# Kernel optimization log

Hardware: AMD Instinct MI355X
Metric: run time of the kernel (lower is better)

## Reference

```python
import jax, jax.numpy as jnp
import numpy as np

B, N, D, H = 4, 2048, 1024, 16
DH = D // H


def setup_inputs() -> dict:
    key = jax.random.key(0)
    ks = jax.random.split(key, 9)
    std = 0.02
    return {
        "x": jax.random.normal(ks[0], (B, N, D), dtype=jnp.float32),
        "Wq": jax.random.normal(ks[1], (D, D), dtype=jnp.float32) * std,
        "bq": jnp.zeros((D,), dtype=jnp.float32),
        "Wk": jax.random.normal(ks[2], (D, D), dtype=jnp.float32) * std,
        "bk": jnp.zeros((D,), dtype=jnp.float32),
        "Wv": jax.random.normal(ks[3], (D, D), dtype=jnp.float32) * std,
        "bv": jnp.zeros((D,), dtype=jnp.float32),
        "Wo": jax.random.normal(ks[4], (D, D), dtype=jnp.float32) * std,
        "bo": jnp.zeros((D,), dtype=jnp.float32),
        "k": 8,
        "dilation": 2,
    }


def _dilated_mask(n_q, n_k, k, dilation):
    # allowed[i, j] = True iff |j - i| <= k*dilation and (j - i) % dilation == 0
    i = jnp.arange(n_q)[:, None]
    j = jnp.arange(n_k)[None, :]
    d = j - i
    return (jnp.abs(d) <= k * dilation) & ((d % dilation) == 0)


def reference(x, Wq, bq, Wk, bk, Wv, bv, Wo, bo, k, dilation):
    b, n_q, d_model = x.shape
    n_heads = H
    d_head = d_model // n_heads
    # self-attention: context = x
    q = (x @ Wq + bq).reshape(b, n_q, n_heads, d_head).transpose(0, 2, 1, 3)  # (B,H,Nq,Dh)
    kk = (x @ Wk + bk).reshape(b, n_q, n_heads, d_head).transpose(0, 2, 1, 3)
    v = (x @ Wv + bv).reshape(b, n_q, n_heads, d_head).transpose(0, 2, 1, 3)

    scale = 1.0 / np.sqrt(d_head).astype(np.float32)
    scores = jnp.einsum("bhqd,bhkd->bhqk", q, kk) * scale  # (B,H,Nq,Nk)
    allowed = _dilated_mask(n_q, n_q, k, dilation)  # (Nq,Nk)
    scores = jnp.where(allowed[None, None], scores, -jnp.inf)
    attn = jax.nn.softmax(scores, axis=-1)
    out = jnp.einsum("bhqk,bhkd->bhqd", attn, v)  # (B,H,Nq,Dh)
    out = out.transpose(0, 2, 1, 3).reshape(b, n_q, d_model)
    return out @ Wo + bo
```

## Files before the change

kernel.cpp:

```cpp
#include <hip/hip_runtime.h>
#include <hip/hip_bf16.h>
#include <hip/hip_fp16.h>
#include <stdint.h>

using bf16 = __hip_bfloat16;

typedef __bf16    bf16x8 __attribute__((ext_vector_type(8)));
typedef float     floatx4 __attribute__((ext_vector_type(4)));
typedef _Float16  f16x8 __attribute__((ext_vector_type(8)));

typedef __attribute__((address_space(3))) void as3_void;
typedef __attribute__((address_space(1))) void as1_void;

#define GLD_LDS16(gp, lp) \
  __builtin_amdgcn_global_load_lds((as1_void*)(uintptr_t)(gp), (as3_void*)(uintptr_t)(lp), 16, 0, 0)

#define FENCE() asm volatile("" ::: "memory")
#define BAR()   do { FENCE(); __builtin_amdgcn_s_barrier(); FENCE(); } while (0)
#define PIN()   __builtin_amdgcn_sched_barrier(0)

__global__ __launch_bounds__(256) void prep_kernel(
    const float* __restrict__ x,
    const float* __restrict__ Wq, const float* __restrict__ Wk,
    const float* __restrict__ Wv, const float* __restrict__ Wo,
    bf16* __restrict__ xbf, bf16* __restrict__ WTqkv, bf16* __restrict__ WoT) {
  __shared__ float tile[64 * 68];
  const int blk = blockIdx.x;
  const int tid = threadIdx.x;
  if (blk < 1024) {
    const int z = blk >> 8, t = blk & 255;
    const float* src = (z == 0) ? Wq : (z == 1) ? Wk : (z == 2) ? Wv : Wo;
    bf16* dst = (z < 3) ? (WTqkv + (size_t)z * 1024 * 1024) : WoT;
    const int nbase = (t & 15) * 64, kbase = (t >> 4) * 64;
    const int r1 = tid >> 4, c1 = tid & 15;
#pragma unroll
    for (int it = 0; it < 4; ++it) {
      const int row = r1 + it * 16;
      const float4 v = *(const float4*)(src + (size_t)(kbase + row) * 1024 + nbase + c1 * 4);
      *(float4*)(tile + row * 68 + c1 * 4) = v;
    }
    __syncthreads();
    const int c2 = tid & 7, n2 = tid >> 3;
#pragma unroll
    for (int it2 = 0; it2 < 2; ++it2) {
      const int n = n2 + it2 * 32;
      bf16 o[8];
#pragma unroll
      for (int s = 0; s < 8; ++s) o[s] = (bf16)tile[(8 * c2 + s) * 68 + n];
      *(uint4*)(dst + (size_t)(nbase + n) * 1024 + kbase + 8 * c2) = *(const uint4*)o;
    }
  } else {
    const size_t basei = ((size_t)(blk - 1024) * 256 + tid) * 16;
#pragma unroll
    for (int h = 0; h < 2; ++h) {
      const float4 a = *(const float4*)(x + basei + h * 8);
      const float4 b = *(const float4*)(x + basei + h * 8 + 4);
      bf16 o[8] = {(bf16)a.x, (bf16)a.y, (bf16)a.z, (bf16)a.w,
                   (bf16)b.x, (bf16)b.y, (bf16)b.z, (bf16)b.w};
      *(uint4*)(xbf + basei + h * 8) = *(const uint4*)o;
    }
  }
}

#define SAU(bufi, u, kt) \
  GLD_LDS16(A + abase + (uint64_t)(u) * 65536 + (uint64_t)(kt) * 64, \
            (char*)Asp[bufi] + (u) * 8192 + ldst)
#define SBU(bufi, u, kt) \
  GLD_LDS16(Bt + bbase + (uint64_t)(u) * 65536 + (uint64_t)(kt) * 64, \
            (char*)Bsp[bufi] + (u) * 8192 + ldst)

#define RDA2(bufi, mb) do { \
    const char* _p = (const char*)Asp[bufi] + (wm * 64 + (mb) * 16 + l16) * 128; \
    af[0][0] = *(const bf16x8*)(_p + pcb0); \
    af[0][1] = *(const bf16x8*)(_p + pcb1); \
    af[1][0] = *(const bf16x8*)(_p + 2048 + pcb0); \
    af[1][1] = *(const bf16x8*)(_p + 2048 + pcb1); \
  } while (0)

#define RDB6(bufi) do { \
    const char* _p = (const char*)Bsp[bufi] + (wn * 96 + l16) * 128; \
    _Pragma("unroll") for (int _j = 0; _j < 6; ++_j) { \
      bfr[_j][0] = *(const bf16x8*)(_p + _j * 2048 + pcb0); \
      bfr[_j][1] = *(const bf16x8*)(_p + _j * 2048 + pcb1); \
    } \
  } while (0)

#define MMQ24(mb) do { \
    _Pragma("unroll") for (int _i = 0; _i < 2; ++_i) \
      _Pragma("unroll") for (int _j = 0; _j < 6; ++_j) \
        _Pragma("unroll") for (int _k = 0; _k < 2; ++_k) \
          acc[(mb) + _i][_j] = __builtin_amdgcn_mfma_f32_16x16x32_bf16( \
              af[_i][_k], bfr[_j][_k], acc[(mb) + _i][_j], 0, 0, 0); \
  } while (0)

__global__ __launch_bounds__(512, 2) void gemm_qkv_8ph(
    const bf16* __restrict__ A, const bf16* __restrict__ Bt,
    const float* __restrict__ b0, const float* __restrict__ b1, const float* __restrict__ b2,
    __half* __restrict__ qkv) {
  const int t    = threadIdx.x;
  const int m0   = blockIdx.x * 256;
  const int n0   = blockIdx.y * 192;
  const int lane = t & 63;
  const int wave = t >> 6;
  const int wm   = wave >> 1;
  const int wn   = wave & 1;
  const int quad = lane >> 4;
  const int l16  = lane & 15;

  __shared__ alignas(16) char smem[114688];
  bf16* const Asp[2] = {(bf16*)smem, (bf16*)(smem + 32768)};
  bf16* const Bsp[2] = {(bf16*)(smem + 65536), (bf16*)(smem + 90112)};

  const int srt = t >> 3;
  const int sct = ((t & 7) ^ (srt & 7)) << 3;
  const uint64_t abase = (uint64_t)(m0 + srt) * 1024 + sct;
  const uint64_t bbase = (uint64_t)(n0 + srt) * 1024 + sct;
  const int ldst = t * 16;

  const int pcb0 = ((quad) ^ (l16 & 7)) << 4;
  const int pcb1 = ((4 + quad) ^ (l16 & 7)) << 4;

  floatx4 acc[4][6];
#pragma unroll
  for (int i = 0; i < 4; ++i)
#pragma unroll
    for (int j = 0; j < 6; ++j) {
      floatx4 z = {0.f, 0.f, 0.f, 0.f};
      acc[i][j] = z;
    }
  bf16x8 af[2][2], bfr[6][2];

  SBU(0, 0, 0); SBU(0, 1, 0); SBU(0, 2, 0);
  SAU(0, 0, 0); SAU(0, 1, 0); SAU(0, 2, 0); SAU(0, 3, 0);
  SBU(1, 0, 1); SBU(1, 1, 1); SBU(1, 2, 1);
  asm volatile("s_waitcnt vmcnt(3)" ::: "memory");
  BAR();

  for (int i = 0; i < 8; ++i) {
    const int kt1 = 2 * i + 1;
    const int kt2 = 2 * i + 2;
    const int kt3 = 2 * i + 3;
    const bool pf = (i < 7);

    RDA2(0, 0); RDB6(0);
    SAU(1, 0, kt1); SAU(1, 1, kt1); SAU(1, 2, kt1); SAU(1, 3, kt1);
    __builtin_amdgcn_s_setprio(1); MMQ24(0); __builtin_amdgcn_s_setprio(0);
    PIN();
    BAR();

    RDA2(0, 2);
    if (pf) { SBU(0, 0, kt2); SBU(0, 1, kt2); SBU(0, 2, kt2); }
    __builtin_amdgcn_s_setprio(1); MMQ24(2); __builtin_amdgcn_s_setprio(0);
    PIN();
    if (pf) { asm volatile("s_waitcnt vmcnt(3)" ::: "memory"); }
    else    { asm volatile("s_waitcnt vmcnt(0)" ::: "memory"); }
    BAR();

    RDA2(1, 0); RDB6(1);
    if (pf) { SAU(0, 0, kt2); SAU(0, 1, kt2); SAU(0, 2, kt2); SAU(0, 3, kt2); }
    __builtin_amdgcn_s_setprio(1); MMQ24(0); __builtin_amdgcn_s_setprio(0);
    PIN();
    BAR();

    RDA2(1, 2);
    if (pf) { SBU(1, 0, kt3); SBU(1, 1, kt3); SBU(1, 2, kt3); }
    __builtin_amdgcn_s_setprio(1); MMQ24(2); __builtin_amdgcn_s_setprio(0);
    PIN();
    if (pf) { asm volatile("s_waitcnt vmcnt(3)" ::: "memory"); }
    BAR();
  }

  float bvs[6];
#pragma unroll
  for (int nj = 0; nj < 6; ++nj) {
    const int n = n0 + wn * 96 + nj * 16 + l16;
    const int which = n >> 10;
    const int c = n & 1023;
    bvs[nj] = ((which == 0) ? b0 : (which == 1) ? b1 : b2)[c];
  }
  _Float16* stg = (_Float16*)smem;
#pragma unroll
  for (int mb = 0; mb < 4; ++mb)
#pragma unroll
    for (int nj = 0; nj < 6; ++nj)
#pragma unroll
      for (int r = 0; r < 4; ++r)
        stg[(wm * 64 + mb * 16 + quad * 4 + r) * 200 + wn * 96 + nj * 16 + l16] =
            (_Float16)(acc[mb][nj][r] + bvs[nj]);
  BAR();
#pragma unroll
  for (int rep = 0; rep < 12; ++rep) {
    const int cc = t + rep * 512;
    const int rl = cc / 24;
    const int ch = cc - rl * 24;
    const f16x8 v = *(const f16x8*)(stg + rl * 200 + ch * 8);
    *(f16x8*)((_Float16*)qkv + (size_t)(m0 + rl) * 3072 + n0 + ch * 8) = v;
  }
}

__global__ __launch_bounds__(256) void gemm_proj(
    const bf16* __restrict__ A, const bf16* __restrict__ Bt,
    const float* __restrict__ bias, float* __restrict__ fout) {
  const int tid  = threadIdx.x;
  const int m0   = blockIdx.x * 128;
  const int n0   = blockIdx.y * 128;
  const int lane = tid & 63;
  const int wave = tid >> 6;
  const int wr   = (wave >> 1) * 64;
  const int wc   = (wave & 1) * 64;
  const int quad = lane >> 4;
  const int l16  = lane & 15;

  __shared__ alignas(16) bf16 As[128 * 64];
  __shared__ alignas(16) bf16 Bs[128 * 64];

  const int srow = tid >> 3;
  const int cg   = (tid & 7) ^ (srow & 7);
  const uint64_t aoff = (uint64_t)(m0 + srow) * 1024 + cg * 8;
  const uint64_t boff = (uint64_t)(n0 + srow) * 1024 + cg * 8;

  floatx4 acc[4][4];
#pragma unroll
  for (int i = 0; i < 4; ++i)
#pragma unroll
    for (int j = 0; j < 4; ++j) {
      floatx4 z = {0.f, 0.f, 0.f, 0.f};
      acc[i][j] = z;
    }

  for (int k0 = 0; k0 < 1024; k0 += 64) {
    __syncthreads();
#pragma unroll
    for (int it = 0; it < 4; ++it) {
      GLD_LDS16(A + aoff + (uint64_t)it * 32768 + k0, (char*)As + it * 4096 + tid * 16);
      GLD_LDS16(Bt + boff + (uint64_t)it * 32768 + k0, (char*)Bs + it * 4096 + tid * 16);
    }
    __syncthreads();

#pragma unroll
    for (int kc = 0; kc < 2; ++kc) {
      bf16x8 af[4], bfr[4];
#pragma unroll
      for (int i = 0; i < 4; ++i) {
        const int mrow = wr + i * 16 + l16;
        const int pca  = (kc * 4 + quad) ^ (mrow & 7);
        af[i] = *(const bf16x8*)(As + mrow * 64 + pca * 8);
        const int nrow = wc + i * 16 + l16;
        const int pcb  = (kc * 4 + quad) ^ (nrow & 7);
        bfr[i] = *(const bf16x8*)(Bs + nrow * 64 + pcb * 8);
      }
#pragma unroll
      for (int i = 0; i < 4; ++i)
#pragma unroll
        for (int j = 0; j < 4; ++j)
          acc[i][j] = __builtin_amdgcn_mfma_f32_16x16x32_bf16(af[i], bfr[j], acc[i][j], 0, 0, 0);
    }
  }

#pragma unroll
  for (int i = 0; i < 4; ++i)
#pragma unroll
    for (int j = 0; j < 4; ++j)
#pragma unroll
      for (int r = 0; r < 4; ++r) {
        const int m = m0 + wr + i * 16 + quad * 4 + r;
        const int n = n0 + wc + j * 16 + l16;
        fout[(uint64_t)m * 1024 + n] = acc[i][j][r] + bias[n];
      }
}

#define RMAXA 32
#define VTS 176
#define PS  104

__global__ __launch_bounds__(256) void dilated_attn_mfma_kernel(
    const __half* __restrict__ qkv, bf16* __restrict__ attn_out,
    const int* __restrict__ kptr, const int* __restrict__ dptr) {
  const int tid  = threadIdx.x;
  const int wave = tid >> 6, lane = tid & 63;
  const int quad = lane >> 4, l16 = lane & 15;
  const int bh = blockIdx.x >> 5;
  const int Q0 = (blockIdx.x & 31) * 64;
  const int b  = bh >> 4, h = bh & 15;
  const int kk  = kptr[0];
  const int dil = dptr[0];
  const int R   = kk * dil;
  const size_t xb = (size_t)b * 2048;
  const int qo = h * 64, ko = 1024 + h * 64, vo = 2048 + h * 64;
  const _Float16* Xh = (const _Float16*)qkv;

  __shared__ alignas(16) _Float16 smem[64 * VTS + 4 * 16 * PS];
  _Float16* VT = smem;
  _Float16* Pw = smem + 64 * VTS + wave * 16 * PS;

  const bool fast = (R <= RMAXA) && (dil >= 1);

  if (fast) {
    {
      const int nch = (64 * VTS + 4 * 16 * PS) / 8;
      const f16x8 z = {0, 0, 0, 0, 0, 0, 0, 0};
      for (int c = tid; c < nch; c += 256) ((f16x8*)smem)[c] = z;
    }
    __syncthreads();

    const int jlo = Q0 - R;
    const int lo = (jlo > 0) ? jlo : 0;
    const int hi = (Q0 + 63 + R < 2047) ? Q0 + 63 + R : 2047;
    const int nrows = hi - lo + 1;
    for (int idx = tid; idx < nrows * 8; idx += 256) {
      const int r = idx >> 3, c = idx & 7;
      const int j = lo + r;
      const f16x8 v = *(const f16x8*)(Xh + (xb + j) * 3072 + vo + c * 8);
      const int col = j - jlo + 32;
#pragma unroll
      for (int s = 0; s < 8; ++s) VT[(c * 8 + s) * VTS + col] = v[s];
    }
    __syncthreads();

    const int i0 = Q0 + wave * 16;
    const f16x8 a0 = *(const f16x8*)(Xh + (xb + i0 + l16) * 3072 + qo + quad * 8);
    const f16x8 a1 = *(const f16x8*)(Xh + (xb + i0 + l16) * 3072 + qo + 32 + quad * 8);

    const int nkt = (16 + 2 * R + 15) >> 4;
    const int jw0 = i0 - R;
    float lsum[4] = {0.f, 0.f, 0.f, 0.f};
    const floatx4 zf = {0.f, 0.f, 0.f, 0.f};

    for (int kt = 0; kt < nkt; ++kt) {
      const int j0 = jw0 + 16 * kt;
      const int jn = j0 + l16;
      const int jc = (jn < 0) ? 0 : (jn > 2047 ? 2047 : jn);
      const f16x8 k0v = *(const f16x8*)(Xh + (xb + jc) * 3072 + ko + quad * 8);
      const f16x8 k1v = *(const f16x8*)(Xh + (xb + jc) * 3072 + ko + 32 + quad * 8);
      floatx4 s4 = __builtin_amdgcn_mfma_f32_16x16x32_f16(a0, k0v, zf, 0, 0, 0);
      s4 = __builtin_amdgcn_mfma_f32_16x16x32_f16(a1, k1v, s4, 0, 0, 0);
#pragma unroll
      for (int r = 0; r < 4; ++r) {
        const int m = quad * 4 + r;
        const int d = jn - (i0 + m);
        const bool valid = ((unsigned)jn < 2048u) && (d >= -R) && (d <= R) && (d % dil == 0);
        const float pe = valid ? __expf(s4[r] * 0.125f) : 0.f;
        lsum[r] += pe;
        Pw[m * PS + kt * 16 + l16] = (_Float16)pe;
      }
    }
#pragma unroll
    for (int r = 0; r < 4; ++r) {
      lsum[r] += __shfl_xor(lsum[r], 1);
      lsum[r] += __shfl_xor(lsum[r], 2);
      lsum[r] += __shfl_xor(lsum[r], 4);
      lsum[r] += __shfl_xor(lsum[r], 8);
    }

    const int nkc = (nkt * 16 + 31) >> 5;
    floatx4 o[4] = {zf, zf, zf, zf};
    const int vbase = 16 * wave + 32;
    for (int c = 0; c < nkc; ++c) {
      const f16x8 pa = *(const f16x8*)(Pw + l16 * PS + c * 32 + quad * 8);
#pragma unroll
      for (int t = 0; t < 4; ++t) {
        const f16x8 vb = *(const f16x8*)(VT + (t * 16 + l16) * VTS + vbase + c * 32 + quad * 8);
        o[t] = __builtin_amdgcn_mfma_f32_16x16x32_f16(pa, vb, o[t], 0, 0, 0);
      }
    }

#pragma unroll
    for (int t = 0; t < 4; ++t) {
#pragma unroll
      for (int r = 0; r < 4; ++r)
        Pw[(quad * 4 + r) * PS + t * 16 + l16] = (_Float16)(o[t][r] / lsum[r]);
    }
    const int orow = lane >> 2, oseg = lane & 3;
#pragma unroll
    for (int hseg = 0; hseg < 2; ++hseg) {
      const f16x8 ov = *(const f16x8*)(Pw + orow * PS + oseg * 16 + hseg * 8);
      bf16 ob[8];
#pragma unroll
      for (int s = 0; s < 8; ++s) ob[s] = (bf16)(float)ov[s];
      *(uint4*)(attn_out + (xb + i0 + orow) * 1024 + h * 64 + oseg * 16 + hseg * 8) =
          *(const uint4*)ob;
    }
    return;
  }

  if (tid < 64) {
    const int i = Q0 + tid;
    float l = 0.f;
    float oacc[64];
#pragma unroll
    for (int u = 0; u < 64; ++u) oacc[u] = 0.f;
    float qv[64];
#pragma unroll
    for (int u = 0; u < 64; ++u) qv[u] = (float)Xh[(xb + i) * 3072 + qo + u];
    for (int tt = -kk; tt <= kk; ++tt) {
      const int j = i + (int)((long long)tt * dil);
      if (j < 0 || j >= 2048) continue;
      float s = 0.f;
      for (int u = 0; u < 64; ++u) s += qv[u] * (float)Xh[(xb + j) * 3072 + ko + u];
      const float pe = __expf(s * 0.125f);
      l += pe;
      for (int u = 0; u < 64; ++u) oacc[u] += pe * (float)Xh[(xb + j) * 3072 + vo + u];
    }
    for (int u = 0; u < 64; ++u)
      attn_out[(xb + i) * 1024 + h * 64 + u] = (bf16)(oacc[u] / l);
  }
}

extern "C" void kernel_launch(void* const* d_in, const int* in_sizes, int n_in,
                              void* d_out, int out_size, void* d_ws, size_t ws_size,
                              hipStream_t stream) {
  const float* x  = (const float*)d_in[0];
  const float* Wq = (const float*)d_in[1];
  const float* bq = (const float*)d_in[2];
  const float* Wk = (const float*)d_in[3];
  const float* bk = (const float*)d_in[4];
  const float* Wv = (const float*)d_in[5];
  const float* bv = (const float*)d_in[6];
  const float* Wo = (const float*)d_in[7];
  const float* bo = (const float*)d_in[8];
  const int* kp   = (const int*)d_in[9];
  const int* dp   = (const int*)d_in[10];
  float* out = (float*)d_out;

  bf16*   xbf   = (bf16*)d_ws;
  bf16*   WTqkv = xbf + 8388608;
  bf16*   WoT   = WTqkv + 3072 * 1024;
  __half* qkv   = (__half*)(WoT + 1024 * 1024);
  bf16*   attnO = xbf;

  prep_kernel<<<dim3(3072), 256, 0, stream>>>(x, Wq, Wk, Wv, Wo, xbf, WTqkv, WoT);

  gemm_qkv_8ph<<<dim3(32, 16), 512, 0, stream>>>(xbf, WTqkv, bq, bk, bv, qkv);

  dilated_attn_mfma_kernel<<<dim3(2048), 256, 0, stream>>>(qkv, attnO, kp, dp);

  gemm_proj<<<dim3(64, 8), 256, 0, stream>>>(attnO, WoT, bo, out);
}
```

Measured before the change: 202.7 us.

## Load QKV GEMM B-operand directly into registers, shrinking LDS to A only

The QKV projection GEMM no longer stages the weight (B) tile through LDS. Each wave loads its 96-column B fragments straight from global memory into double-buffered registers, while A is still streamed into LDS via global_load_lds. The main loop becomes a simpler two-stage k-step with one barrier per step. The epilogue is split into two 128-row passes so the fp16 staging fits in the smaller 64 KB shared buffer. The aim is to cut LDS footprint and LDS read traffic, possibly allowing more blocks per CU. The cost is more VGPRs for B buffers, uncoalesced-ish per-lane global reads of B duplicated across the four wm waves, and an extra barrier pair in the epilogue.

```diff
diff --git a/kernel.cpp b/kernel.cpp
--- a/kernel.cpp
+++ b/kernel.cpp
@@ -17,7 +17,6 @@
 
 #define FENCE() asm volatile("" ::: "memory")
 #define BAR()   do { FENCE(); __builtin_amdgcn_s_barrier(); FENCE(); } while (0)
-#define PIN()   __builtin_amdgcn_sched_barrier(0)
 
 __global__ __launch_bounds__(256) void prep_kernel(
     const float* __restrict__ x,
@@ -65,32 +64,33 @@
 #define SAU(bufi, u, kt) \
   GLD_LDS16(A + abase + (uint64_t)(u) * 65536 + (uint64_t)(kt) * 64, \
             (char*)Asp[bufi] + (u) * 8192 + ldst)
-#define SBU(bufi, u, kt) \
-  GLD_LDS16(Bt + bbase + (uint64_t)(u) * 65536 + (uint64_t)(kt) * 64, \
-            (char*)Bsp[bufi] + (u) * 8192 + ldst)
-
-#define RDA2(bufi, mb) do { \
-    const char* _p = (const char*)Asp[bufi] + (wm * 64 + (mb) * 16 + l16) * 128; \
-    af[0][0] = *(const bf16x8*)(_p + pcb0); \
-    af[0][1] = *(const bf16x8*)(_p + pcb1); \
-    af[1][0] = *(const bf16x8*)(_p + 2048 + pcb0); \
-    af[1][1] = *(const bf16x8*)(_p + 2048 + pcb1); \
-  } while (0)
-
-#define RDB6(bufi) do { \
-    const char* _p = (const char*)Bsp[bufi] + (wn * 96 + l16) * 128; \
-    _Pragma("unroll") for (int _j = 0; _j < 6; ++_j) { \
-      bfr[_j][0] = *(const bf16x8*)(_p + _j * 2048 + pcb0); \
-      bfr[_j][1] = *(const bf16x8*)(_p + _j * 2048 + pcb1); \
+
+#define LDB12(bN, kt) do { \
+    _Pragma("unroll") for (int _jb = 0; _jb < 6; ++_jb) { \
+      bN[_jb][0] = *(const bf16x8*)(Bt + bof + (uint64_t)_jb * 16384 + (uint64_t)(kt) * 64); \
+      bN[_jb][1] = *(const bf16x8*)(Bt + bof + (uint64_t)_jb * 16384 + (uint64_t)(kt) * 64 + 32); \
     } \
   } while (0)
 
-#define MMQ24(mb) do { \
-    _Pragma("unroll") for (int _i = 0; _i < 2; ++_i) \
-      _Pragma("unroll") for (int _j = 0; _j < 6; ++_j) \
-        _Pragma("unroll") for (int _k = 0; _k < 2; ++_k) \
-          acc[(mb) + _i][_j] = __builtin_amdgcn_mfma_f32_16x16x32_bf16( \
-              af[_i][_k], bfr[_j][_k], acc[(mb) + _i][_j], 0, 0, 0); \
+#define KSTEP(curb, nxtb, bC, bN, ti, islast) do { \
+    asm volatile("s_waitcnt vmcnt(12)" ::: "memory"); \
+    BAR(); \
+    if (!(islast)) { \
+      SAU(nxtb, 0, (ti) + 1); SAU(nxtb, 1, (ti) + 1); \
+      SAU(nxtb, 2, (ti) + 1); SAU(nxtb, 3, (ti) + 1); \
+      LDB12(bN, (ti) + 1); \
+    } \
+    _Pragma("unroll") for (int _mb = 0; _mb < 4; ++_mb) { \
+      const char* _p = (const char*)Asp[curb] + (wm * 64 + _mb * 16 + l16) * 128; \
+      const bf16x8 _a0 = *(const bf16x8*)(_p + pcb0); \
+      const bf16x8 _a1 = *(const bf16x8*)(_p + pcb1); \
+      __builtin_amdgcn_s_setprio(1); \
+      _Pragma("unroll") for (int _j = 0; _j < 6; ++_j) { \
+        acc[_mb][_j] = __builtin_amdgcn_mfma_f32_16x16x32_bf16(_a0, bC[_j][0], acc[_mb][_j], 0, 0, 0); \
+        acc[_mb][_j] = __builtin_amdgcn_mfma_f32_16x16x32_bf16(_a1, bC[_j][1], acc[_mb][_j], 0, 0, 0); \
+      } \
+      __builtin_amdgcn_s_setprio(0); \
+    } \
   } while (0)
 
 __global__ __launch_bounds__(512, 2) void gemm_qkv_8ph(
@@ -107,15 +107,15 @@
   const int quad = lane >> 4;
   const int l16  = lane & 15;
 
-  __shared__ alignas(16) char smem[114688];
+  __shared__ alignas(16) char smem[65536];
   bf16* const Asp[2] = {(bf16*)smem, (bf16*)(smem + 32768)};
-  bf16* const Bsp[2] = {(bf16*)(smem + 65536), (bf16*)(smem + 90112)};
 
   const int srt = t >> 3;
   const int sct = ((t & 7) ^ (srt & 7)) << 3;
   const uint64_t abase = (uint64_t)(m0 + srt) * 1024 + sct;
-  const uint64_t bbase = (uint64_t)(n0 + srt) * 1024 + sct;
   const int ldst = t * 16;
+
+  const uint64_t bof = (uint64_t)(n0 + wn * 96 + l16) * 1024 + quad * 8;
 
   const int pcb0 = ((quad) ^ (l16 & 7)) << 4;
   const int pcb1 = ((4 + quad) ^ (l16 & 7)) << 4;
@@ -128,46 +128,15 @@
       floatx4 z = {0.f, 0.f, 0.f, 0.f};
       acc[i][j] = z;
     }
-  bf16x8 af[2][2], bfr[6][2];
-
-  SBU(0, 0, 0); SBU(0, 1, 0); SBU(0, 2, 0);
+  bf16x8 bregA[6][2], bregB[6][2];
+
   SAU(0, 0, 0); SAU(0, 1, 0); SAU(0, 2, 0); SAU(0, 3, 0);
-  SBU(1, 0, 1); SBU(1, 1, 1); SBU(1, 2, 1);
-  asm volatile("s_waitcnt vmcnt(3)" ::: "memory");
-  BAR();
-
-  for (int i = 0; i < 8; ++i) {
-    const int kt1 = 2 * i + 1;
-    const int kt2 = 2 * i + 2;
-    const int kt3 = 2 * i + 3;
-    const bool pf = (i < 7);
-
-    RDA2(0, 0); RDB6(0);
-    SAU(1, 0, kt1); SAU(1, 1, kt1); SAU(1, 2, kt1); SAU(1, 3, kt1);
-    __builtin_amdgcn_s_setprio(1); MMQ24(0); __builtin_amdgcn_s_setprio(0);
-    PIN();
-    BAR();
-
-    RDA2(0, 2);
-    if (pf) { SBU(0, 0, kt2); SBU(0, 1, kt2); SBU(0, 2, kt2); }
-    __builtin_amdgcn_s_setprio(1); MMQ24(2); __builtin_amdgcn_s_setprio(0);
-    PIN();
-    if (pf) { asm volatile("s_waitcnt vmcnt(3)" ::: "memory"); }
-    else    { asm volatile("s_waitcnt vmcnt(0)" ::: "memory"); }
-    BAR();
-
-    RDA2(1, 0); RDB6(1);
-    if (pf) { SAU(0, 0, kt2); SAU(0, 1, kt2); SAU(0, 2, kt2); SAU(0, 3, kt2); }
-    __builtin_amdgcn_s_setprio(1); MMQ24(0); __builtin_amdgcn_s_setprio(0);
-    PIN();
-    BAR();
-
-    RDA2(1, 2);
-    if (pf) { SBU(1, 0, kt3); SBU(1, 1, kt3); SBU(1, 2, kt3); }
-    __builtin_amdgcn_s_setprio(1); MMQ24(2); __builtin_amdgcn_s_setprio(0);
-    PIN();
-    if (pf) { asm volatile("s_waitcnt vmcnt(3)" ::: "memory"); }
-    BAR();
+  LDB12(bregA, 0);
+
+#pragma unroll 1
+  for (int ii = 0; ii < 8; ++ii) {
+    KSTEP(0, 1, bregA, bregB, 2 * ii, false);
+    KSTEP(1, 0, bregB, bregA, 2 * ii + 1, (ii == 7));
   }
 
   float bvs[6];
@@ -180,21 +149,28 @@
   }
   _Float16* stg = (_Float16*)smem;
 #pragma unroll
-  for (int mb = 0; mb < 4; ++mb)
-#pragma unroll
-    for (int nj = 0; nj < 6; ++nj)
-#pragma unroll
-      for (int r = 0; r < 4; ++r)
-        stg[(wm * 64 + mb * 16 + quad * 4 + r) * 200 + wn * 96 + nj * 16 + l16] =
-            (_Float16)(acc[mb][nj][r] + bvs[nj]);
-  BAR();
-#pragma unroll
-  for (int rep = 0; rep < 12; ++rep) {
-    const int cc = t + rep * 512;
-    const int rl = cc / 24;
-    const int ch = cc - rl * 24;
-    const f16x8 v = *(const f16x8*)(stg + rl * 200 + ch * 8);
-    *(f16x8*)((_Float16*)qkv + (size_t)(m0 + rl) * 3072 + n0 + ch * 8) = v;
+  for (int p = 0; p < 2; ++p) {
+    BAR();
+    if ((wm >> 1) == p) {
+      const int lr0 = (wm & 1) * 64;
+#pragma unroll
+      for (int mb = 0; mb < 4; ++mb)
+#pragma unroll
+        for (int nj = 0; nj < 6; ++nj)
+#pragma unroll
+          for (int r = 0; r < 4; ++r)
+            stg[(lr0 + mb * 16 + quad * 4 + r) * 200 + wn * 96 + nj * 16 + l16] =
+                (_Float16)(acc[mb][nj][r] + bvs[nj]);
+    }
+    BAR();
+#pragma unroll
+    for (int rep = 0; rep < 6; ++rep) {
+      const int cc = t + rep * 512;
+      const int rl = cc / 24;
+      const int ch = cc - rl * 24;
+      const f16x8 v = *(const f16x8*)(stg + rl * 200 + ch * 8);
+      *(f16x8*)((_Float16*)qkv + (size_t)(m0 + p * 128 + rl) * 3072 + n0 + ch * 8) = v;
+    }
   }
 }
 
```

Result: slower. 269.9 us (+33.1%).

## Rewrite output projection GEMM with 256x128 tiles and double-buffered LDS pipeline

Applied to the files above, without the earlier changes.

Replaces the simple single-buffered output projection GEMM with an 8-wave, 256x128-tile kernel. It double-buffers A and B in LDS through direct global-to-LDS loads, interleaves prefetch of the next K-tiles with the MFMA work, and uses s_setprio around the MFMA blocks. The aim is to hide global load latency and halve the number of blocks. In exchange it uses 96KB of LDS per block, which limits occupancy, and it relies on carefully hand-counted vmcnt waits.

```diff
diff --git a/kernel.cpp b/kernel.cpp
--- a/kernel.cpp
+++ b/kernel.cpp
@@ -198,26 +198,62 @@
   }
 }
 
-__global__ __launch_bounds__(256) void gemm_proj(
+#define PSAU(bufi, u, kt) \
+  GLD_LDS16(A + pab + (uint64_t)(u) * 65536 + (uint64_t)(kt) * 64, \
+            (char*)PAs[bufi] + (u) * 8192 + ldst)
+#define PSBU(bufi, u, kt) \
+  GLD_LDS16(Bt + pbb + (uint64_t)(u) * 65536 + (uint64_t)(kt) * 64, \
+            (char*)PBs[bufi] + (u) * 8192 + ldst)
+
+#define PRDA(bufi, mb) do { \
+    const char* _p = (const char*)PAs[bufi] + (wm * 64 + (mb) * 16 + l16) * 128; \
+    af[0][0] = *(const bf16x8*)(_p + pcb0); \
+    af[0][1] = *(const bf16x8*)(_p + pcb1); \
+    af[1][0] = *(const bf16x8*)(_p + 2048 + pcb0); \
+    af[1][1] = *(const bf16x8*)(_p + 2048 + pcb1); \
+  } while (0)
+
+#define PRDB(bufi) do { \
+    const char* _p = (const char*)PBs[bufi] + (wn * 64 + l16) * 128; \
+    _Pragma("unroll") for (int _j = 0; _j < 4; ++_j) { \
+      bfr[_j][0] = *(const bf16x8*)(_p + _j * 2048 + pcb0); \
+      bfr[_j][1] = *(const bf16x8*)(_p + _j * 2048 + pcb1); \
+    } \
+  } while (0)
+
+#define PMM16(mb) do { \
+    _Pragma("unroll") for (int _i = 0; _i < 2; ++_i) \
+      _Pragma("unroll") for (int _j = 0; _j < 4; ++_j) \
+        _Pragma("unroll") for (int _k = 0; _k < 2; ++_k) \
+          acc[(mb) + _i][_j] = __builtin_amdgcn_mfma_f32_16x16x32_bf16( \
+              af[_i][_k], bfr[_j][_k], acc[(mb) + _i][_j], 0, 0, 0); \
+  } while (0)
+
+__global__ __launch_bounds__(512, 2) void gemm_proj(
     const bf16* __restrict__ A, const bf16* __restrict__ Bt,
     const float* __restrict__ bias, float* __restrict__ fout) {
-  const int tid  = threadIdx.x;
-  const int m0   = blockIdx.x * 128;
+  const int t    = threadIdx.x;
+  const int m0   = blockIdx.x * 256;
   const int n0   = blockIdx.y * 128;
-  const int lane = tid & 63;
-  const int wave = tid >> 6;
-  const int wr   = (wave >> 1) * 64;
-  const int wc   = (wave & 1) * 64;
+  const int lane = t & 63;
+  const int wave = t >> 6;
+  const int wm   = wave >> 1;
+  const int wn   = wave & 1;
   const int quad = lane >> 4;
   const int l16  = lane & 15;
 
-  __shared__ alignas(16) bf16 As[128 * 64];
-  __shared__ alignas(16) bf16 Bs[128 * 64];
-
-  const int srow = tid >> 3;
-  const int cg   = (tid & 7) ^ (srow & 7);
-  const uint64_t aoff = (uint64_t)(m0 + srow) * 1024 + cg * 8;
-  const uint64_t boff = (uint64_t)(n0 + srow) * 1024 + cg * 8;
+  __shared__ alignas(16) char smem[98304];
+  bf16* const PAs[2] = {(bf16*)smem, (bf16*)(smem + 32768)};
+  bf16* const PBs[2] = {(bf16*)(smem + 65536), (bf16*)(smem + 81920)};
+
+  const int srt = t >> 3;
+  const int sct = ((t & 7) ^ (srt & 7)) << 3;
+  const uint64_t pab = (uint64_t)(m0 + srt) * 1024 + sct;
+  const uint64_t pbb = (uint64_t)(n0 + srt) * 1024 + sct;
+  const int ldst = t * 16;
+
+  const int pcb0 = ((quad) ^ (l16 & 7)) << 4;
+  const int pcb1 = ((4 + quad) ^ (l16 & 7)) << 4;
 
   floatx4 acc[4][4];
 #pragma unroll
@@ -227,45 +263,61 @@
       floatx4 z = {0.f, 0.f, 0.f, 0.f};
       acc[i][j] = z;
     }
-
-  for (int k0 = 0; k0 < 1024; k0 += 64) {
-    __syncthreads();
-#pragma unroll
-    for (int it = 0; it < 4; ++it) {
-      GLD_LDS16(A + aoff + (uint64_t)it * 32768 + k0, (char*)As + it * 4096 + tid * 16);
-      GLD_LDS16(Bt + boff + (uint64_t)it * 32768 + k0, (char*)Bs + it * 4096 + tid * 16);
-    }
-    __syncthreads();
-
-#pragma unroll
-    for (int kc = 0; kc < 2; ++kc) {
-      bf16x8 af[4], bfr[4];
-#pragma unroll
-      for (int i = 0; i < 4; ++i) {
-        const int mrow = wr + i * 16 + l16;
-        const int pca  = (kc * 4 + quad) ^ (mrow & 7);
-        af[i] = *(const bf16x8*)(As + mrow * 64 + pca * 8);
-        const int nrow = wc + i * 16 + l16;
-        const int pcb  = (kc * 4 + quad) ^ (nrow & 7);
-        bfr[i] = *(const bf16x8*)(Bs + nrow * 64 + pcb * 8);
-      }
-#pragma unroll
-      for (int i = 0; i < 4; ++i)
-#pragma unroll
-        for (int j = 0; j < 4; ++j)
-          acc[i][j] = __builtin_amdgcn_mfma_f32_16x16x32_bf16(af[i], bfr[j], acc[i][j], 0, 0, 0);
-    }
-  }
-
-#pragma unroll
-  for (int i = 0; i < 4; ++i)
-#pragma unroll
-    for (int j = 0; j < 4; ++j)
+  bf16x8 af[2][2], bfr[4][2];
+
+  PSBU(0, 0, 0); PSBU(0, 1, 0);
+  PSAU(0, 0, 0); PSAU(0, 1, 0); PSAU(0, 2, 0); PSAU(0, 3, 0);
+  PSBU(1, 0, 1); PSBU(1, 1, 1);
+  asm volatile("s_waitcnt vmcnt(2)" ::: "memory");
+  BAR();
+
+  for (int i = 0; i < 8; ++i) {
+    const int kt1 = 2 * i + 1;
+    const int kt2 = 2 * i + 2;
+    const int kt3 = 2 * i + 3;
+    const bool pf = (i < 7);
+
+    PRDA(0, 0); PRDB(0);
+    PSAU(1, 0, kt1); PSAU(1, 1, kt1); PSAU(1, 2, kt1); PSAU(1, 3, kt1);
+    __builtin_amdgcn_s_setprio(1); PMM16(0); __builtin_amdgcn_s_setprio(0);
+    PIN();
+    BAR();
+
+    PRDA(0, 2);
+    if (pf) { PSBU(0, 0, kt2); PSBU(0, 1, kt2); }
+    __builtin_amdgcn_s_setprio(1); PMM16(2); __builtin_amdgcn_s_setprio(0);
+    PIN();
+    if (pf) { asm volatile("s_waitcnt vmcnt(2)" ::: "memory"); }
+    else    { asm volatile("s_waitcnt vmcnt(0)" ::: "memory"); }
+    BAR();
+
+    PRDA(1, 0); PRDB(1);
+    if (pf) { PSAU(0, 0, kt2); PSAU(0, 1, kt2); PSAU(0, 2, kt2); PSAU(0, 3, kt2); }
+    __builtin_amdgcn_s_setprio(1); PMM16(0); __builtin_amdgcn_s_setprio(0);
+    PIN();
+    BAR();
+
+    PRDA(1, 2);
+    if (pf) { PSBU(1, 0, kt3); PSBU(1, 1, kt3); }
+    __builtin_amdgcn_s_setprio(1); PMM16(2); __builtin_amdgcn_s_setprio(0);
+    PIN();
+    if (pf) { asm volatile("s_waitcnt vmcnt(2)" ::: "memory"); }
+    BAR();
+  }
+
+  float bvs[4];
+#pragma unroll
+  for (int nj = 0; nj < 4; ++nj)
+    bvs[nj] = bias[n0 + wn * 64 + nj * 16 + l16];
+#pragma unroll
+  for (int mb = 0; mb < 4; ++mb)
+#pragma unroll
+    for (int nj = 0; nj < 4; ++nj)
 #pragma unroll
       for (int r = 0; r < 4; ++r) {
-        const int m = m0 + wr + i * 16 + quad * 4 + r;
-        const int n = n0 + wc + j * 16 + l16;
-        fout[(uint64_t)m * 1024 + n] = acc[i][j][r] + bias[n];
+        const int m = m0 + wm * 64 + mb * 16 + quad * 4 + r;
+        const int n = n0 + wn * 64 + nj * 16 + l16;
+        fout[(uint64_t)m * 1024 + n] = acc[mb][nj][r] + bvs[nj];
       }
 }
 
@@ -434,5 +486,5 @@
 
   dilated_attn_mfma_kernel<<<dim3(2048), 256, 0, stream>>>(qkv, attnO, kp, dp);
 
-  gemm_proj<<<dim3(64, 8), 256, 0, stream>>>(attnO, WoT, bo, out);
+  gemm_proj<<<dim3(32, 8), 512, 0, stream>>>(attnO, WoT, bo, out);
 }
```

After: 207.6 us. 1.02x slower.
